# Optimization experiments

Measured on AMD Instinct MI355X. Metric: run time of the kernel, lower is better.

## Reference

```python
import jax, jax.numpy as jnp
import numpy as np

N = 100000
EPS = 1e-5
DROPOUT_P = 0.5


def sage_conv(x, src, dst, Wl, Wr, b):
    # mean aggregation of source features onto destination nodes (PyG SAGEConv)
    agg = jax.ops.segment_sum(x[src], dst, num_segments=N)           # [N, d]
    deg = jax.ops.segment_sum(jnp.ones(src.shape, x.dtype), dst, num_segments=N)
    mean = agg / jnp.maximum(deg, 1.0)[:, None]
    return mean @ Wl + x @ Wr + b                                     # lin_l(aggr) + lin_r(x)


def batch_norm(x, gamma, beta):
    mu = jnp.mean(x, axis=0)
    var = jnp.mean((x - mu) ** 2, axis=0)  # biased var (training-mode BN)
    return gamma * (x - mu) * jax.lax.rsqrt(var + EPS) + beta


def dropout(x, key):
    keep = jax.random.bernoulli(key, 1.0 - DROPOUT_P, x.shape)
    return jnp.where(keep, x / (1.0 - DROPOUT_P), 0.0)


def setup_inputs() -> dict:
    key = jax.random.key(0)
    ks = jax.random.split(key, 16)
    d_in, d_h, d_out = 128, 128, 16
    E = 1600000
    def w(k, i, o):
        return jax.random.normal(k, (i, o), jnp.float32) / np.sqrt(i)
    x = jax.random.normal(ks[0], (N, d_in), jnp.float32)
    edge_index = jax.random.randint(ks[1], (2, E), 0, N, jnp.int32)
    return {
        'x': x,
        'edge_index': edge_index,
        'W1l': w(ks[2], d_in, d_h), 'W1r': w(ks[3], d_in, d_h), 'b1': jnp.zeros((d_h,), jnp.float32),
        'g1': jnp.ones((d_h,), jnp.float32), 'be1': jnp.zeros((d_h,), jnp.float32),
        'W2l': w(ks[4], d_h, d_h), 'W2r': w(ks[5], d_h, d_h), 'b2': jnp.zeros((d_h,), jnp.float32),
        'g2': jnp.ones((d_h,), jnp.float32), 'be2': jnp.zeros((d_h,), jnp.float32),
        'W3l': w(ks[6], d_h, d_out), 'W3r': w(ks[7], d_h, d_out), 'b3': jnp.zeros((d_out,), jnp.float32),
    }


def reference(x, edge_index, W1l, W1r, b1, g1, be1, W2l, W2r, b2, g2, be2, W3l, W3r, b3):
    src, dst = edge_index[0], edge_index[1]
    k1, k2 = jax.random.split(jax.random.key(42))
    h = jax.nn.relu(batch_norm(sage_conv(x, src, dst, W1l, W1r, b1), g1, be1))
    h = dropout(h, k1)
    h = jax.nn.relu(batch_norm(sage_conv(h, src, dst, W2l, W2r, b2), g2, be2))
    h = dropout(h, k2)
    return sage_conv(h, src, dst, W3l, W3r, b3)
```

## Files before the change

kernel.cpp:

```cpp
#include <hip/hip_runtime.h>
#include <cstdint>
#include <cstddef>

#define THREADS 256

typedef __attribute__((ext_vector_type(8))) short bf16x8;
typedef __attribute__((ext_vector_type(4))) float f32x4;
typedef __attribute__((ext_vector_type(2))) float f32x2;

__host__ __device__ __forceinline__ void tf2x32(unsigned k0, unsigned k1,
                                                unsigned x0, unsigned x1,
                                                unsigned* o0, unsigned* o1) {
  unsigned ks2 = k0 ^ k1 ^ 0x1BD11BDAu;
  x0 += k0; x1 += k1;
#define TFR(r) { x0 += x1; x1 = (x1 << (r)) | (x1 >> (32 - (r))); x1 ^= x0; }
  TFR(13) TFR(15) TFR(26) TFR(6)   x0 += k1;  x1 += ks2 + 1u;
  TFR(17) TFR(29) TFR(16) TFR(24)  x0 += ks2; x1 += k0 + 2u;
  TFR(13) TFR(15) TFR(26) TFR(6)   x0 += k0;  x1 += k1 + 3u;
  TFR(17) TFR(29) TFR(16) TFR(24)  x0 += k1;  x1 += ks2 + 4u;
  TFR(13) TFR(15) TFR(26) TFR(6)   x0 += ks2; x1 += k0 + 5u;
#undef TFR
  *o0 = x0; *o1 = x1;
}

__device__ __forceinline__ unsigned f2bf(float f) {
  unsigned b = __float_as_uint(f);
  return (b + 0x7fffu + ((b >> 16) & 1u)) >> 16;
}

__device__ __forceinline__ unsigned char f2fp8(float f) {
  return (unsigned char)(__builtin_amdgcn_cvt_pk_fp8_f32(f, f, 0, false) & 0xff);
}

__device__ __forceinline__ void bn_mask8(float* v, const float* __restrict__ scsh,
                                         int col0, unsigned e, unsigned o) {
  float sc[8], sh[8];
  *(float4*)&sc[0] = *(const float4*)(scsh + col0);
  *(float4*)&sc[4] = *(const float4*)(scsh + col0 + 4);
  *(float4*)&sh[0] = *(const float4*)(scsh + 128 + col0);
  *(float4*)&sh[4] = *(const float4*)(scsh + 128 + col0 + 4);
#pragma unroll
  for (int p = 0; p < 4; ++p) {
    float t0 = fmaxf(v[2 * p] * sc[2 * p] + sh[2 * p], 0.f);
    float t1 = fmaxf(v[2 * p + 1] * sc[2 * p + 1] + sh[2 * p + 1], 0.f);
    v[2 * p] = ((e >> p) & 1u) ? 2.f * t0 : 0.f;
    v[2 * p + 1] = ((o >> p) & 1u) ? 2.f * t1 : 0.f;
  }
}

__global__ __launch_bounds__(THREADS) void compute_deg(const int* __restrict__ dst,
                                                       int* __restrict__ deg, int E) {
  int e = blockIdx.x * THREADS + threadIdx.x;
  if (e < E) atomicAdd(&deg[dst[e]], 1);
}

__global__ __launch_bounds__(THREADS) void bin_edges2(const int* __restrict__ src,
                                                      const int* __restrict__ dst,
                                                      unsigned* __restrict__ bcnt,
                                                      unsigned* __restrict__ buckets,
                                                      int cap, int nbk,
                                                      int E, int e8, unsigned nmax) {
  int g = blockIdx.x & 7;
  int chunk = blockIdx.x >> 3;
  int nchunk = gridDim.x >> 3;
  int lo = g * e8;
  int hi = lo + e8; if (hi > E) hi = E;
  unsigned* mycnt = bcnt + (size_t)g * nbk * 8;
  unsigned* mybkt = buckets + (size_t)g * nbk * cap;
  int stride = nchunk * THREADS * 4;
  for (int e0 = lo + (chunk * THREADS + threadIdx.x) * 4; e0 < hi; e0 += stride) {
    if (e0 + 4 <= hi) {
      int4 d4 = *(const int4*)(dst + e0);
      int4 s4 = *(const int4*)(src + e0);
      int dd[4] = {d4.x, d4.y, d4.z, d4.w};
      int ss[4] = {s4.x, s4.y, s4.z, s4.w};
#pragma unroll
      for (int j = 0; j < 4; ++j) {
        unsigned d = (unsigned)dd[j];
        if (d >= nmax) continue;
        int b = d >> 7;
        unsigned p = atomicAdd(&mycnt[(size_t)b * 8], 1u);
        if (p < (unsigned)cap)
          mybkt[(size_t)b * cap + p] = ((d & 127u) << 17) | (unsigned)ss[j];
      }
    } else {
      for (int e = e0; e < hi; ++e) {
        unsigned d = (unsigned)dst[e];
        if (d >= nmax) continue;
        int b = d >> 7;
        unsigned p = atomicAdd(&mycnt[(size_t)b * 8], 1u);
        if (p < (unsigned)cap)
          mybkt[(size_t)b * cap + p] = ((d & 127u) << 17) | (unsigned)src[e];
      }
    }
  }
}

__global__ __launch_bounds__(1024) void scan_buckets(const unsigned* __restrict__ bcnt,
                                                     int* __restrict__ bbase,
                                                     int cap, int nbk) {
  __shared__ int sdata[1024];
  int t = threadIdx.x;
  int tot = 0;
  if (t < nbk) {
#pragma unroll
    for (int g = 0; g < 8; ++g) {
      int c = (int)bcnt[((size_t)g * nbk + t) * 8];
      tot += (c > cap) ? cap : c;
    }
  }
  sdata[t] = tot;
  __syncthreads();
  for (int off = 1; off < 1024; off <<= 1) {
    int v = (t >= off) ? sdata[t - off] : 0;
    __syncthreads();
    sdata[t] += v;
    __syncthreads();
  }
  if (t < nbk) bbase[t] = sdata[t] - tot;
  if (t == nbk - 1) bbase[nbk] = sdata[t];
}

#define BCAP_LDS 6144
__global__ __launch_bounds__(THREADS) void scatter_csr2(
    const unsigned* __restrict__ buckets, const unsigned* __restrict__ bcnt,
    const int* __restrict__ bbase, int* __restrict__ deg, int* __restrict__ start,
    int* __restrict__ colbuf, int cap, int nbk, int N) {
  __shared__ unsigned img[BCAP_LDS];
  __shared__ int cnt[128], scanv[128], cnt2[128];
  int b = blockIdx.x;
  int t = threadIdx.x;
  if (t < 128) { cnt[t] = 0; cnt2[t] = 0; }
  __syncthreads();
  for (int g = 0; g < 8; ++g) {
    int mg = (int)bcnt[((size_t)g * nbk + b) * 8]; if (mg > cap) mg = cap;
    const unsigned* bk = buckets + ((size_t)g * nbk + b) * cap;
    for (int i = t; i < mg; i += THREADS)
      atomicAdd(&cnt[(bk[i] >> 17) & 127], 1);
  }
  __syncthreads();
  if (t < 128) scanv[t] = cnt[t];
  __syncthreads();
  for (int off = 1; off < 128; off <<= 1) {
    int v = 0;
    if (t < 128 && t >= off) v = scanv[t - off];
    __syncthreads();
    if (t < 128) scanv[t] += v;
    __syncthreads();
  }
  int segbase = bbase[b];
  int seglen = bbase[b + 1] - segbase;
  if (t < 128) {
    int node = (b << 7) + t;
    if (node < N) {
      deg[node] = cnt[t];
      start[node] = segbase + scanv[t] - cnt[t];
    }
  }
  __syncthreads();
  bool fits = (seglen <= BCAP_LDS);
  for (int g = 0; g < 8; ++g) {
    int mg = (int)bcnt[((size_t)g * nbk + b) * 8]; if (mg > cap) mg = cap;
    const unsigned* bk = buckets + ((size_t)g * nbk + b) * cap;
    for (int i = t; i < mg; i += THREADS) {
      unsigned v = bk[i];
      int dl = (v >> 17) & 127;
      int pos = scanv[dl] - cnt[dl] + atomicAdd(&cnt2[dl], 1);
      if (fits) {
        if (pos >= 0 && pos < BCAP_LDS) img[pos] = v & 0x1FFFFu;
      } else {
        colbuf[segbase + pos] = (int)(v & 0x1FFFFu);
      }
    }
  }
  __syncthreads();
  if (fits) {
    for (int i = t; i < seglen; i += THREADS)
      colbuf[segbase + i] = (int)img[i];
  }
}

__global__ __launch_bounds__(THREADS) void scan1_local(const int* __restrict__ deg,
                                                       int* __restrict__ start,
                                                       int* __restrict__ blksum, int n) {
  __shared__ int sdata[THREADS];
  int i = blockIdx.x * THREADS + threadIdx.x;
  int d = (i < n) ? deg[i] : 0;
  sdata[threadIdx.x] = d;
  __syncthreads();
  for (int off = 1; off < THREADS; off <<= 1) {
    int v = (threadIdx.x >= off) ? sdata[threadIdx.x - off] : 0;
    __syncthreads();
    sdata[threadIdx.x] += v;
    __syncthreads();
  }
  if (i < n) start[i] = sdata[threadIdx.x] - d;
  if (threadIdx.x == THREADS - 1) blksum[blockIdx.x] = sdata[THREADS - 1];
}

__global__ __launch_bounds__(512) void scan2_blocks(const int* __restrict__ blksum,
                                                    int* __restrict__ blkbase, int nb) {
  __shared__ int sdata[512];
  int t = threadIdx.x;
  int v = (t < nb) ? blksum[t] : 0;
  sdata[t] = v;
  __syncthreads();
  for (int off = 1; off < 512; off <<= 1) {
    int u = (t >= off) ? sdata[t - off] : 0;
    __syncthreads();
    sdata[t] += u;
    __syncthreads();
  }
  if (t < nb) blkbase[t] = sdata[t] - v;
}

__global__ __launch_bounds__(THREADS) void scan3_add(int* __restrict__ start,
                                                     const int* __restrict__ blkbase,
                                                     int n) {
  int i = blockIdx.x * THREADS + threadIdx.x;
  if (i < n) start[i] += blkbase[blockIdx.x];
}

__global__ __launch_bounds__(THREADS) void fill_csr_xcd(const int* __restrict__ src,
                                                        const int* __restrict__ dst,
                                                        const int* __restrict__ start,
                                                        int* __restrict__ fill,
                                                        int* __restrict__ colbuf,
                                                        int E, int rngw) {
  int g = blockIdx.x & 7;
  int chunk = blockIdx.x >> 3;
  int nchunk = gridDim.x >> 3;
  int lo = g * rngw, hi = lo + rngw;
  int stride = nchunk * THREADS;
  for (int e = chunk * THREADS + threadIdx.x; e < E; e += stride) {
    int d = dst[e];
    if (d >= lo && d < hi) {
      int p = atomicAdd(&fill[d], 1);
      colbuf[start[d] + p] = src[e];
    }
  }
}

__global__ __launch_bounds__(THREADS) void pack_weights(const float* __restrict__ Wl,
                                                        const float* __restrict__ Wr,
                                                        uint4* __restrict__ Wp) {
  int idx = blockIdx.x * THREADS + threadIdx.x;
  int n = idx & 15, quad = (idx >> 4) & 3, kc = (idx >> 6) & 3, nt = idx >> 8;
  const float* W = (nt < 8) ? Wl : Wr;
  int col = ((nt & 7) * 16) + n;
  int k0 = kc * 32 + quad * 8;
  unsigned u[4];
#pragma unroll
  for (int p = 0; p < 4; ++p) {
    unsigned lo = f2bf(W[(size_t)(k0 + 2 * p) * 128 + col]);
    unsigned hi = f2bf(W[(size_t)(k0 + 2 * p + 1) * 128 + col]);
    u[p] = lo | (hi << 16);
  }
  Wp[idx] = make_uint4(u[0], u[1], u[2], u[3]);
}

template <int FUSE>
__global__ __launch_bounds__(THREADS) void gemm_dual_mfma(
    const float* A, const uint4* __restrict__ Wp, const float* __restrict__ bias,
    const float* __restrict__ scsh, const unsigned long long* __restrict__ mask,
    unsigned char* __restrict__ Cl, float* __restrict__ Cr, int M) {
  int t = threadIdx.x;
  int wv = t >> 6;
  int lane = t & 63;
  int m16 = lane & 15;
  int quad = lane >> 4;
  int arow = blockIdx.x * 64 + wv * 16 + m16;
  bool avalid = arow < M;

  union U8 { uint4 u; bf16x8 v; };

  unsigned long long m0 = 0, m1 = 0;
  if (FUSE && avalid) {
    m0 = mask[2 * (size_t)arow];
    m1 = mask[2 * (size_t)arow + 1];
  }

  bf16x8 af[4];
  const float* ap = A + (size_t)arow * 128 + quad * 8;
#pragma unroll
  for (int kc = 0; kc < 4; ++kc) {
    float v[8] = {0.f, 0.f, 0.f, 0.f, 0.f, 0.f, 0.f, 0.f};
    if (avalid) {
      *(float4*)&v[0] = *(const float4*)(ap + kc * 32);
      *(float4*)&v[4] = *(const float4*)(ap + kc * 32 + 4);
    }
    if (FUSE) {
      int col0 = kc * 32 + quad * 8;
      int shift = (col0 >> 1);
      unsigned e = (unsigned)(m0 >> shift) & 0xFu;
      unsigned o = (unsigned)(m1 >> shift) & 0xFu;
      bn_mask8(v, scsh, col0, e, o);
    }
    U8 u;
    u.u.x = f2bf(v[0]) | (f2bf(v[1]) << 16);
    u.u.y = f2bf(v[2]) | (f2bf(v[3]) << 16);
    u.u.z = f2bf(v[4]) | (f2bf(v[5]) << 16);
    u.u.w = f2bf(v[6]) | (f2bf(v[7]) << 16);
    af[kc] = u.v;
  }

  int orow0 = blockIdx.x * 64 + wv * 16 + quad * 4;
  const uint4* wp = Wp + m16;

  {
    f32x4 acc[8];
#pragma unroll
    for (int i = 0; i < 8; ++i) acc[i] = (f32x4){0.f, 0.f, 0.f, 0.f};
#pragma unroll
    for (int nt = 0; nt < 8; ++nt) {
#pragma unroll
      for (int kc = 0; kc < 4; ++kc) {
        U8 b;
        b.u = wp[((nt * 4 + kc) * 4 + quad) * 16];
        acc[nt] = __builtin_amdgcn_mfma_f32_16x16x32_bf16(af[kc], b.v, acc[nt], 0, 0, 0);
      }
    }
#pragma unroll
    for (int nt = 0; nt < 8; ++nt) {
      int col = nt * 16 + m16;
#pragma unroll
      for (int r = 0; r < 4; ++r) {
        int row = orow0 + r;
        if (row < M) Cl[(size_t)row * 128 + col] = f2fp8(acc[nt][r]);
      }
    }
  }

  {
    f32x4 acc[8];
#pragma unroll
    for (int i = 0; i < 8; ++i) acc[i] = (f32x4){0.f, 0.f, 0.f, 0.f};
#pragma unroll
    for (int nt = 0; nt < 8; ++nt) {
#pragma unroll
      for (int kc = 0; kc < 4; ++kc) {
        U8 b;
        b.u = wp[(((nt + 8) * 4 + kc) * 4 + quad) * 16];
        acc[nt] = __builtin_amdgcn_mfma_f32_16x16x32_bf16(af[kc], b.v, acc[nt], 0, 0, 0);
      }
    }
#pragma unroll
    for (int nt = 0; nt < 8; ++nt) {
      int col = nt * 16 + m16;
      float bb = bias[col];
#pragma unroll
      for (int r = 0; r < 4; ++r) {
        int row = orow0 + r;
        if (row < M) Cr[(size_t)row * 128 + col] = acc[nt][r] + bb;
      }
    }
  }
}

__global__ __launch_bounds__(THREADS) void gemm16_dual(const float* __restrict__ A,
                                                       const float* __restrict__ Wl,
                                                       const float* __restrict__ Wr,
                                                       const float* __restrict__ br,
                                                       const float* __restrict__ scsh,
                                                       const unsigned long long* __restrict__ mask,
                                                       unsigned short* __restrict__ Cl,
                                                       float* __restrict__ Cr, int M) {
  __shared__ __align__(16) float Wls[128][16];
  __shared__ __align__(16) float Wrs[128][16];
  __shared__ __align__(16) float As[16][130];
  int t = threadIdx.x;
#pragma unroll
  for (int i = 0; i < 2; ++i) {
    int lin = (t + i * THREADS) << 2;
    *(float4*)&Wls[0][lin & 2047] = *(const float4*)(Wl + lin);
    *(float4*)&Wrs[0][lin & 2047] = *(const float4*)(Wr + lin);
  }
  int row0 = blockIdx.x * 16;
  int r = t >> 4;
  int c = t & 15;
  {
    int grow = row0 + r;
    float v[8] = {0.f, 0.f, 0.f, 0.f, 0.f, 0.f, 0.f, 0.f};
    if (grow < M) {
      const float* ap = A + (size_t)grow * 128 + c * 8;
      *(float4*)&v[0] = *(const float4*)(ap);
      *(float4*)&v[4] = *(const float4*)(ap + 4);
      unsigned long long m0 = mask[2 * (size_t)grow];
      unsigned long long m1 = mask[2 * (size_t)grow + 1];
      int shift = c * 4;
      unsigned e = (unsigned)(m0 >> shift) & 0xFu;
      unsigned o = (unsigned)(m1 >> shift) & 0xFu;
      bn_mask8(v, scsh, c * 8, e, o);
    }
    *(float4*)&As[r][c * 8] = *(float4*)&v[0];
    *(float4*)&As[r][c * 8 + 4] = *(float4*)&v[4];
  }
  __syncthreads();
  float accl = 0.f, accr = 0.f;
#pragma unroll 4
  for (int k = 0; k < 128; ++k) {
    float a = As[r][k];
    accl += a * Wls[k][c];
    accr += a * Wrs[k][c];
  }
  int grow = row0 + r;
  if (grow < M) {
    Cl[(size_t)grow * 16 + c] = (unsigned short)f2bf(accl);
    Cr[(size_t)grow * 16 + c] = accr + br[c];
  }
}

__global__ __launch_bounds__(THREADS) void aggregate128_fp8(
    const unsigned char* __restrict__ Y, float* __restrict__ Z,
    const int* __restrict__ colbuf, const int* __restrict__ start,
    const int* __restrict__ deg, unsigned long long* __restrict__ mask,
    unsigned mk0, unsigned mk1, int nnodes) {
  int w = (blockIdx.x * THREADS + threadIdx.x) >> 6;
  int lane = threadIdx.x & 63;
  if (w >= nnodes) return;
  unsigned a0, a1, b0, b1;
  unsigned ib = (unsigned)w * 128u + (unsigned)(lane << 1);
  tf2x32(mk0, mk1, 0u, ib, &a0, &a1);
  tf2x32(mk0, mk1, 0u, ib + 1u, &b0, &b1);
  bool kp0 = ((a0 ^ a1) >> 31) == 0u;
  bool kp1 = ((b0 ^ b1) >> 31) == 0u;

  int half = lane >> 5;
  int l32 = lane & 31;
  const int* cb = colbuf + start[w];
  int dg = deg[w];
  const unsigned char* yp = Y + (l32 << 2);
  float a0f = 0.f, a1f = 0.f, a2f = 0.f, a3f = 0.f;
  int i = 0;
#define ACC(u) { \
    f32x2 lo = __builtin_amdgcn_cvt_pk_f32_fp8((int)(u), false); \
    f32x2 hi = __builtin_amdgcn_cvt_pk_f32_fp8((int)(u), true);  \
    a0f += lo.x; a1f += lo.y; a2f += hi.x; a3f += hi.y; }
  for (; i + 8 <= dg; i += 8) {
    int e0 = cb[i + half], e1 = cb[i + 2 + half];
    int e2 = cb[i + 4 + half], e3 = cb[i + 6 + half];
    unsigned u0 = *(const unsigned*)(yp + (size_t)e0 * 128);
    unsigned u1 = *(const unsigned*)(yp + (size_t)e1 * 128);
    unsigned u2 = *(const unsigned*)(yp + (size_t)e2 * 128);
    unsigned u3 = *(const unsigned*)(yp + (size_t)e3 * 128);
    ACC(u0) ACC(u1) ACC(u2) ACC(u3)
  }
  for (; i + 2 <= dg; i += 2) {
    int e0 = cb[i + half];
    unsigned u0 = *(const unsigned*)(yp + (size_t)e0 * 128);
    ACC(u0)
  }
  if (i < dg) {
    int e0 = cb[i];
    unsigned u0 = *(const unsigned*)(yp + (size_t)e0 * 128);
    if (half == 0) { ACC(u0) }
  }
#undef ACC
  a0f += __shfl(a0f, lane + 32);
  a1f += __shfl(a1f, lane + 32);
  a2f += __shfl(a2f, lane + 32);
  a3f += __shfl(a3f, lane + 32);

  unsigned long long bm0 = __ballot(kp0);
  unsigned long long bm1 = __ballot(kp1);
  if (lane == 0) {
    mask[2 * (size_t)w] = bm0;
    mask[2 * (size_t)w + 1] = bm1;
  }
  if (half == 0) {
    float sc = 1.0f / fmaxf((float)dg, 1.0f);
    float* zp = Z + (size_t)w * 128 + (l32 << 2);
    float4 z = *(const float4*)zp;
    z.x += a0f * sc;
    z.y += a1f * sc;
    z.z += a2f * sc;
    z.w += a3f * sc;
    *(float4*)zp = z;
  }
}

__global__ __launch_bounds__(THREADS) void aggregate16_bf16(
    const unsigned short* __restrict__ Y, float* __restrict__ Out,
    const int* __restrict__ colbuf, const int* __restrict__ start,
    const int* __restrict__ deg, int nnodes) {
  int gid = blockIdx.x * THREADS + threadIdx.x;
  int n = gid >> 3;
  int cp = gid & 7;
  if (n >= nnodes) return;
  const int* cb = colbuf + start[n];
  int dg = deg[n];
  const unsigned short* yp = Y + (cp << 1);
  float ax = 0.f, ay = 0.f;
  int i = 0;
  for (; i + 8 <= dg; i += 8) {
    int e[8];
#pragma unroll
    for (int j = 0; j < 8; ++j) e[j] = cb[i + j];
    unsigned u[8];
#pragma unroll
    for (int j = 0; j < 8; ++j) u[j] = *(const unsigned*)(yp + (size_t)e[j] * 16);
#pragma unroll
    for (int j = 0; j < 8; ++j) {
      ax += __uint_as_float(u[j] << 16);
      ay += __uint_as_float(u[j] & 0xffff0000u);
    }
  }
  for (; i < dg; ++i) {
    unsigned u = *(const unsigned*)(yp + (size_t)cb[i] * 16);
    ax += __uint_as_float(u << 16);
    ay += __uint_as_float(u & 0xffff0000u);
  }
  float sc = 1.0f / fmaxf((float)dg, 1.0f);
  size_t off = (size_t)n * 16 + (cp << 1);
  float2 o = *(const float2*)(Out + off);
  o.x += ax * sc;
  o.y += ay * sc;
  *(float2*)(Out + off) = o;
}

__global__ __launch_bounds__(THREADS) void bn_stats(const float* __restrict__ H,
                                                    float* __restrict__ sums, int n) {
  int col = threadIdx.x & 127;
  int half = threadIdx.x >> 7;
  float s = 0.f, sq = 0.f;
  for (int r = blockIdx.x * 2 + half; r < n; r += gridDim.x * 2) {
    float v = H[(size_t)r * 128 + col];
    s += v;
    sq += v * v;
  }
  __shared__ float ls[THREADS], lq[THREADS];
  ls[threadIdx.x] = s;
  lq[threadIdx.x] = sq;
  __syncthreads();
  if (half == 0) {
    s += ls[col + 128];
    sq += lq[col + 128];
    atomicAdd(&sums[col], s);
    atomicAdd(&sums[128 + col], sq);
  }
}

__global__ void bn_finalize(const float* __restrict__ sums,
                            const float* __restrict__ g,
                            const float* __restrict__ be,
                            float* __restrict__ scsh, float n) {
  int c = threadIdx.x;
  float mu = sums[c] / n;
  float var = sums[128 + c] / n - mu * mu;
  float inv = rsqrtf(var + 1e-5f);
  float sc = g[c] * inv;
  scsh[c] = sc;
  scsh[128 + c] = be[c] - mu * sc;
}

extern "C" void kernel_launch(void* const* d_in, const int* in_sizes, int n_in,
                              void* d_out, int out_size, void* d_ws, size_t ws_size,
                              hipStream_t stream) {
  const float* x   = (const float*)d_in[0];
  const int* eidx  = (const int*)d_in[1];
  const float* W1l = (const float*)d_in[2];
  const float* W1r = (const float*)d_in[3];
  const float* b1  = (const float*)d_in[4];
  const float* g1  = (const float*)d_in[5];
  const float* be1 = (const float*)d_in[6];
  const float* W2l = (const float*)d_in[7];
  const float* W2r = (const float*)d_in[8];
  const float* b2  = (const float*)d_in[9];
  const float* g2  = (const float*)d_in[10];
  const float* be2 = (const float*)d_in[11];
  const float* W3l = (const float*)d_in[12];
  const float* W3r = (const float*)d_in[13];
  const float* b3  = (const float*)d_in[14];
  float* out = (float*)d_out;

  const int N = in_sizes[0] / 128;
  const int E = in_sizes[1] / 2;
  const int* esrc = eidx;
  const int* edst = eidx + E;

  size_t N128 = (size_t)N * 128;
  size_t Nw = ((size_t)N + 63) & ~(size_t)63;
  size_t Ew = ((size_t)E + 63) & ~(size_t)63;

  float* sums1 = (float*)d_ws;
  float* sums2 = sums1 + 256;
  int* ideg    = (int*)(sums2 + 256);
  int* ifill   = ideg + N;
  int* istart  = ifill + N;
  int* iblksum = istart + (int)Nw;
  int* iblkbase = iblksum + 512;
  int* bbase   = iblkbase + 512;
  float* scsh1 = (float*)(bbase + 1088);
  float* scsh2 = scsh1 + 256;
  uint4* wp1 = (uint4*)(scsh2 + 256);
  uint4* wp2 = wp1 + 4096;
  unsigned long long* mask1 = (unsigned long long*)(wp2 + 4096);
  unsigned long long* mask2 = mask1 + 2 * Nw;
  int* icol  = (int*)(mask2 + 2 * Nw);
  unsigned char* buf0b = (unsigned char*)(icol + Ew);
  unsigned short* buf0h = (unsigned short*)buf0b;
  float* buf1 = (float*)(buf0b + ((N128 + 255) & ~(size_t)255));

  unsigned* buckets = (unsigned*)buf0b;
  int nbk = (N + 127) >> 7;
  int bcap = 1024;
  size_t bucket_bytes = (size_t)8 * nbk * bcap * 4;
  size_t bufregion_bytes = ((N128 + 255) & ~(size_t)255) + 4 * N128;
  bool newcsr = (N <= 131072) && (nbk <= 1023) &&
                ((size_t)64 * nbk <= (size_t)N) &&
                (bucket_bytes <= bufregion_bytes);

  unsigned k1a, k1b, k2a, k2b;
  tf2x32(0u, 42u, 0u, 0u, &k1a, &k1b);
  tf2x32(0u, 42u, 0u, 1u, &k2a, &k2b);

  hipMemsetAsync(sums1, 0, (512 + 2 * (size_t)N) * 4, stream);

  pack_weights<<<16, THREADS, 0, stream>>>(W1l, W1r, wp1);
  pack_weights<<<16, THREADS, 0, stream>>>(W2l, W2r, wp2);

  int gN = (N + THREADS - 1) / THREADS;
  if (newcsr) {
    int e8 = (((E + 7) / 8) + 3) & ~3;
    bin_edges2<<<2048, THREADS, 0, stream>>>(esrc, edst, (unsigned*)ifill,
                                             buckets, bcap, nbk, E, e8,
                                             (unsigned)N);
    scan_buckets<<<1, 1024, 0, stream>>>((const unsigned*)ifill, bbase,
                                         bcap, nbk);
    scatter_csr2<<<nbk, THREADS, 0, stream>>>(buckets, (const unsigned*)ifill,
                                              bbase, ideg, istart, icol,
                                              bcap, nbk, N);
  } else {
    int gE = (E + THREADS - 1) / THREADS;
    compute_deg<<<gE, THREADS, 0, stream>>>(edst, ideg, E);
    scan1_local<<<gN, THREADS, 0, stream>>>(ideg, istart, iblksum, N);
    scan2_blocks<<<1, 512, 0, stream>>>(iblksum, iblkbase, gN);
    scan3_add<<<gN, THREADS, 0, stream>>>(istart, iblkbase, N);
    int rngw = (N + 7) / 8;
    fill_csr_xcd<<<2048, THREADS, 0, stream>>>(esrc, edst, istart, ifill, icol, E, rngw);
  }

  int gM64 = (N + 63) / 64;
  int gW = (N + 3) / 4;
  int gA16 = (N * 8 + THREADS - 1) / THREADS;
  float nf = (float)N;

  gemm_dual_mfma<0><<<gM64, THREADS, 0, stream>>>(x, wp1, b1, nullptr, nullptr,
                                                  buf0b, buf1, N);
  aggregate128_fp8<<<gW, THREADS, 0, stream>>>(buf0b, buf1, icol, istart, ideg,
                                               mask1, k1a, k1b, N);
  bn_stats<<<1024, THREADS, 0, stream>>>(buf1, sums1, N);
  bn_finalize<<<1, 128, 0, stream>>>(sums1, g1, be1, scsh1, nf);

  gemm_dual_mfma<1><<<gM64, THREADS, 0, stream>>>(buf1, wp2, b2, scsh1, mask1,
                                                  buf0b, buf1, N);
  aggregate128_fp8<<<gW, THREADS, 0, stream>>>(buf0b, buf1, icol, istart, ideg,
                                               mask2, k2a, k2b, N);
  bn_stats<<<1024, THREADS, 0, stream>>>(buf1, sums2, N);
  bn_finalize<<<1, 128, 0, stream>>>(sums2, g2, be2, scsh2, nf);

  gemm16_dual<<<(N + 15) / 16, THREADS, 0, stream>>>(buf1, W3l, W3r, b3, scsh2,
                                                     mask2, buf0h, out, N);
  aggregate16_bf16<<<gA16, THREADS, 0, stream>>>(buf0h, out, icol, istart, ideg, N);
}
```

Before: 562.6 us.

## Bin edges via shared-memory histogram and locally sorted tile writes

Replaces per-edge global atomics in the edge-binning kernel with a per-tile LDS histogram, a block-wide prefix scan, and one global atomic per nonempty bucket per tile. Edges are first staged into a bucket-sorted image in shared memory, then written to global buckets so neighbouring threads write neighbouring addresses. This removes global atomic contention and scattered writes, at the cost of extra barriers, re-reading dst/src, a serial scan, and fewer blocks (512).

Result: faster. 513.7 us (-8.7%).

```diff
diff --git a/kernel.cpp b/kernel.cpp
--- a/kernel.cpp
+++ b/kernel.cpp
@@ -54,12 +54,19 @@
   if (e < E) atomicAdd(&deg[dst[e]], 1);
 }
 
-__global__ __launch_bounds__(THREADS) void bin_edges2(const int* __restrict__ src,
-                                                      const int* __restrict__ dst,
-                                                      unsigned* __restrict__ bcnt,
-                                                      unsigned* __restrict__ buckets,
-                                                      int cap, int nbk,
-                                                      int E, int e8, unsigned nmax) {
+#define BIN_TILE 4096
+#define EPT 16
+__global__ __launch_bounds__(THREADS) void bin_edges3(
+    const int* __restrict__ src, const int* __restrict__ dst,
+    unsigned* __restrict__ bcnt, unsigned* __restrict__ buckets,
+    int cap, int nbk, int E, int e8, unsigned nmax) {
+  __shared__ unsigned hist[1024];
+  __shared__ unsigned lofs[1024];
+  __shared__ unsigned gbase[1024];
+  __shared__ unsigned part[THREADS];
+  __shared__ unsigned img[BIN_TILE];
+  __shared__ unsigned opos[BIN_TILE];
+  __shared__ int s_total;
   int g = blockIdx.x & 7;
   int chunk = blockIdx.x >> 3;
   int nchunk = gridDim.x >> 3;
@@ -67,32 +74,61 @@
   int hi = lo + e8; if (hi > E) hi = E;
   unsigned* mycnt = bcnt + (size_t)g * nbk * 8;
   unsigned* mybkt = buckets + (size_t)g * nbk * cap;
-  int stride = nchunk * THREADS * 4;
-  for (int e0 = lo + (chunk * THREADS + threadIdx.x) * 4; e0 < hi; e0 += stride) {
-    if (e0 + 4 <= hi) {
-      int4 d4 = *(const int4*)(dst + e0);
-      int4 s4 = *(const int4*)(src + e0);
-      int dd[4] = {d4.x, d4.y, d4.z, d4.w};
-      int ss[4] = {s4.x, s4.y, s4.z, s4.w};
-#pragma unroll
-      for (int j = 0; j < 4; ++j) {
-        unsigned d = (unsigned)dd[j];
-        if (d >= nmax) continue;
+  int t = threadIdx.x;
+  for (int tile = lo + chunk * BIN_TILE; tile < hi; tile += nchunk * BIN_TILE) {
+    for (int i = t; i < 1024; i += THREADS) hist[i] = 0;
+    __syncthreads();
+    unsigned l[EPT];
+#pragma unroll
+    for (int j = 0; j < EPT; ++j) {
+      int e = tile + j * THREADS + t;
+      l[j] = 0xFFFFFFFFu;
+      if (e < hi) {
+        unsigned d = (unsigned)dst[e];
+        if (d < nmax) l[j] = atomicAdd(&hist[d >> 7], 1u);
+      }
+    }
+    __syncthreads();
+    unsigned c0 = hist[t * 4], c1 = hist[t * 4 + 1];
+    unsigned c2 = hist[t * 4 + 2], c3 = hist[t * 4 + 3];
+    part[t] = c0 + c1 + c2 + c3;
+    __syncthreads();
+    for (int off = 1; off < THREADS; off <<= 1) {
+      unsigned v = (t >= off) ? part[t - off] : 0u;
+      __syncthreads();
+      part[t] += v;
+      __syncthreads();
+    }
+    unsigned run = (t > 0) ? part[t - 1] : 0u;
+    lofs[t * 4] = run; run += c0;
+    lofs[t * 4 + 1] = run; run += c1;
+    lofs[t * 4 + 2] = run; run += c2;
+    lofs[t * 4 + 3] = run;
+    for (int b = t; b < nbk; b += THREADS) {
+      unsigned c = hist[b];
+      if (c) gbase[b] = atomicAdd(&mycnt[(size_t)b * 8], c);
+    }
+    if (t == 0) s_total = (int)part[THREADS - 1];
+    __syncthreads();
+#pragma unroll
+    for (int j = 0; j < EPT; ++j) {
+      if (l[j] != 0xFFFFFFFFu) {
+        int e = tile + j * THREADS + t;
+        unsigned d = (unsigned)dst[e];
+        unsigned s = (unsigned)src[e];
         int b = d >> 7;
-        unsigned p = atomicAdd(&mycnt[(size_t)b * 8], 1u);
-        if (p < (unsigned)cap)
-          mybkt[(size_t)b * cap + p] = ((d & 127u) << 17) | (unsigned)ss[j];
+        unsigned sidx = lofs[b] + l[j];
+        img[sidx] = ((d & 127u) << 17) | s;
+        unsigned gp = gbase[b] + l[j];
+        opos[sidx] = (gp < (unsigned)cap) ? (unsigned)b * cap + gp : 0xFFFFFFFFu;
       }
-    } else {
-      for (int e = e0; e < hi; ++e) {
-        unsigned d = (unsigned)dst[e];
-        if (d >= nmax) continue;
-        int b = d >> 7;
-        unsigned p = atomicAdd(&mycnt[(size_t)b * 8], 1u);
-        if (p < (unsigned)cap)
-          mybkt[(size_t)b * cap + p] = ((d & 127u) << 17) | (unsigned)src[e];
-      }
-    }
+    }
+    __syncthreads();
+    for (int i = t; i < s_total; i += THREADS) {
+      unsigned op = opos[i];
+      if (op != 0xFFFFFFFFu) mybkt[op] = img[i];
+    }
+    __syncthreads();
   }
 }
 
@@ -622,9 +658,9 @@
   int gN = (N + THREADS - 1) / THREADS;
   if (newcsr) {
     int e8 = (((E + 7) / 8) + 3) & ~3;
-    bin_edges2<<<2048, THREADS, 0, stream>>>(esrc, edst, (unsigned*)ifill,
-                                             buckets, bcap, nbk, E, e8,
-                                             (unsigned)N);
+    bin_edges3<<<512, THREADS, 0, stream>>>(esrc, edst, (unsigned*)ifill,
+                                            buckets, bcap, nbk, E, e8,
+                                            (unsigned)N);
     scan_buckets<<<1, 1024, 0, stream>>>((const unsigned*)ifill, bbase,
                                          bcap, nbk);
     scatter_csr2<<<nbk, THREADS, 0, stream>>>(buckets, (const unsigned*)ifill,
```
